# Optimization experiments

Hardware: AMD Instinct MI355X
Metric: run time of the kernel (lower is better)

## Reference

```python
import jax, jax.numpy as jnp
import numpy as np

RADIUS = 3.0  # suppression radius in meters (init kwarg `radius`)


def _radius_nms(x, y, valid, radius):
    """Greedy radius NMS over points in index order.
    x, y: [N] coordinates; valid: [N] bool (point belongs to this class).
    Returns keep mask [N]: point kept iff valid and not within `radius` of
    any previously kept point.
    """
    N = x.shape[0]
    r2 = radius * radius

    def step(supp, i):
        keep = valid[i] & jnp.logical_not(supp[i])
        d2 = (x - x[i]) ** 2 + (y - y[i]) ** 2  # [N]
        supp = supp | (keep & (d2 <= r2))
        return supp, keep

    _, keeps = jax.lax.scan(step, jnp.zeros(N, dtype=bool), jnp.arange(N))
    return keeps


def setup_inputs() -> dict:
    key = jax.random.key(0)
    k1, k2 = jax.random.split(key)
    B, C, W, H, CL = 4, 4, 64, 128, 5
    segmented_channels = jax.random.normal(k1, (B, C, W, H), dtype=jnp.float32)
    # lidar channels 0,1 are x,y point coordinates (meters); scale for realism
    lidar = jax.random.normal(k2, (B, CL, W, H), dtype=jnp.float32) * 30.0
    return {"segmented_channels": segmented_channels, "lidar": lidar}


def reference(segmented_channels, lidar):
    B, C, W, H = segmented_channels.shape
    N = W * H
    # val, ind = segmented_channels.max(dim=1) -> per-pixel predicted class
    ind = jnp.argmax(segmented_channels, axis=1).reshape(B, N)  # [B, N] int
    x = lidar[:, 0].reshape(B, N)  # [B, N]
    y = lidar[:, 1].reshape(B, N)
    # classes 1 .. C-1 (class 0 = background, skipped in the loop)
    classes = jnp.arange(1, C)
    valid = ind[:, None, :] == classes[None, :, None]  # [B, C-1, N] bool
    # vmap greedy NMS over classes, then over batch (x,y shared across classes)
    nms_c = jax.vmap(_radius_nms, in_axes=(None, None, 0, None))
    nms_bc = jax.vmap(nms_c, in_axes=(0, 0, 0, None))
    keep = nms_bc(x, y, valid, RADIUS)  # [B, C-1, N] bool
    # dense (padded) stand-in for the ragged per-class kept point lists:
    # kept coordinates where keep, zeros elsewhere
    coords = jnp.stack([x, y], axis=-1)  # [B, N, 2]
    kept_coords = coords[:, None, :, :] * keep[..., None].astype(coords.dtype)  # [B, C-1, N, 2]
    return kept_coords, keep
```

## Files before the change

kernel.cpp:

```cpp
#include <hip/hip_runtime.h>
#include <cstdint>


#define NPTS 8192
#define CAP  2560
#define R2C  9.0f
#define GW   60
#define GORG 126.0f
#define GINV 0.23809524f
#define GMAXC 59.0f

__global__ __launch_bounds__(1024) void radius_nms_kernel(
    const float* __restrict__ seg,
    const float* __restrict__ lidar,
    float* __restrict__ out)
{
#pragma clang fp contract(off)
    const int bx   = blockIdx.x;
    const int b    = bx / 3;
    const int cls  = (bx % 3) + 1;
    const int tid  = threadIdx.x;
    const int lane = tid & 63;
    const int wv   = tid >> 6;

    __shared__ float2 xy[CAP + 1];
    __shared__ unsigned short oidx[CAP];
    __shared__ unsigned long long keptW[CAP / 64];
    __shared__ int waveTot[16];
    __shared__ unsigned short slots[GW * GW * 4];
    __shared__ unsigned int cnt32[(GW * GW + 3) / 4];

    float* out0 = out + (size_t)bx * NPTS * 2;
    float* out1 = out + 196608 + (size_t)bx * NPTS;

    for (int i = tid; i < NPTS * 2; i += 1024) out0[i] = 0.0f;
    for (int i = tid; i < NPTS; i += 1024) out1[i] = 0.0f;
    for (int i = tid; i < GW * GW * 2; i += 1024)
        ((unsigned*)slots)[i] = ((unsigned)CAP << 16) | (unsigned)CAP;
    for (int i = tid; i < (GW * GW + 3) / 4; i += 1024) cnt32[i] = 0u;
    if (tid == 0) xy[CAP] = make_float2(3.0e38f, 3.0e38f);

    const float* segb = seg + (size_t)b * 4 * NPTS;
    const float* lx   = lidar + (size_t)b * 5 * NPTS;
    const float* ly   = lx + NPTS;

    float px[8], py[8];
    int flags = 0, cnt = 0;
    const int n0 = tid * 8;
#pragma unroll
    for (int k = 0; k < 8; ++k) {
        const int n = n0 + k;
        float v0 = segb[n];
        float v1 = segb[NPTS + n];
        float v2 = segb[2 * NPTS + n];
        float v3 = segb[3 * NPTS + n];
        int bi = 0; float bv = v0;
        if (v1 > bv) { bv = v1; bi = 1; }
        if (v2 > bv) { bv = v2; bi = 2; }
        if (v3 > bv) { bv = v3; bi = 3; }
        px[k] = lx[n];
        py[k] = ly[n];
        if (bi == cls) { flags |= (1 << k); ++cnt; }
    }

    int v = cnt;
    for (int off = 1; off < 64; off <<= 1) {
        int nv = __shfl_up(v, off, 64);
        if (lane >= off) v += nv;
    }
    if (lane == 63) waveTot[wv] = v;
    __syncthreads();
    if (wv == 0) {
        int t = (lane < 16) ? waveTot[lane] : 0;
        for (int off = 1; off < 16; off <<= 1) {
            int nt = __shfl_up(t, off, 64);
            if (lane >= off) t += nt;
        }
        if (lane < 16) waveTot[lane] = t;
    }
    __syncthreads();

    int M = waveTot[15];
    if (M > CAP) M = CAP;
    int base = ((wv == 0) ? 0 : waveTot[wv - 1]) + v - cnt;
#pragma unroll
    for (int k = 0; k < 8; ++k) {
        if (flags & (1 << k)) {
            if (base < CAP) {
                xy[base] = make_float2(px[k], py[k]);
                oidx[base] = (unsigned short)(n0 + k);
            }
            ++base;
        }
    }
    __syncthreads();

    if (wv == 0) {
        const int ntiles = (M + 63) >> 6;
        for (int t = 0; t < ntiles; ++t) {
            const int ts = t << 6;
            const int p  = ts + lane;
            float qx = 3.0e38f, qy = 3.0e38f;
            if (p < M) { float2 q = xy[p]; qx = q.x; qy = q.y; }

            float fx = floorf((qx + GORG) * GINV);
            fx = fminf(fmaxf(fx, 0.0f), GMAXC);
            float fy = floorf((qy + GORG) * GINV);
            fy = fminf(fmaxf(fy, 0.0f), GMAXC);
            const int cx = (int)fx, cy = (int)fy;

            const int cxm = (cx > 0) ? cx - 1 : 0;
            const int cxp = (cx < GW - 1) ? cx + 1 : GW - 1;
            const int rm  = ((cy > 0) ? cy - 1 : 0) * GW;
            const int r0  = cy * GW;
            const int rp  = ((cy < GW - 1) ? cy + 1 : GW - 1) * GW;

            unsigned long long sw[9];
            sw[0] = *(const unsigned long long*)&slots[(rm + cxm) * 4];
            sw[1] = *(const unsigned long long*)&slots[(rm + cx ) * 4];
            sw[2] = *(const unsigned long long*)&slots[(rm + cxp) * 4];
            sw[3] = *(const unsigned long long*)&slots[(r0 + cxm) * 4];
            sw[4] = *(const unsigned long long*)&slots[(r0 + cx ) * 4];
            sw[5] = *(const unsigned long long*)&slots[(r0 + cxp) * 4];
            sw[6] = *(const unsigned long long*)&slots[(rp + cxm) * 4];
            sw[7] = *(const unsigned long long*)&slots[(rp + cx ) * 4];
            sw[8] = *(const unsigned long long*)&slots[(rp + cxp) * 4];

            bool sup = false;
#pragma unroll
            for (int i = 0; i < 9; ++i) {
                unsigned long long w = sw[i];
#pragma unroll
                for (int k = 0; k < 4; ++k) {
                    int idx = (int)((w >> (16 * k)) & 0xFFFFull);
                    float2 r = xy[idx];
                    float dx = qx - r.x;
                    float dy = qy - r.y;
                    sup |= (dx * dx + dy * dy) <= R2C;
                }
            }

            int cntT = M - ts; if (cntT > 64) cntT = 64;
            unsigned long long tm =
                (cntT >= 64) ? ~0ull : ((1ull << cntT) - 1ull);
            unsigned long long alive = __ballot(!sup) & tm;
            unsigned long long keepm = 0ull;
            while (alive) {
                const int l = __builtin_ctzll(alive);
                const float xl = __int_as_float(
                    __builtin_amdgcn_readlane(__float_as_int(qx), l));
                const float yl = __int_as_float(
                    __builtin_amdgcn_readlane(__float_as_int(qy), l));
                const float dx = qx - xl;
                const float dy = qy - yl;
                unsigned long long b2 = __ballot((dx * dx + dy * dy) <= R2C);
                keepm |= (1ull << l);
                alive &= ~b2;
            }
            if (lane == 0) keptW[t] = keepm;

            if ((keepm >> lane) & 1ull) {
                const int c = cy * GW + cx;
                const unsigned sh = 8u * (unsigned)(c & 3);
                unsigned old = atomicAdd(&cnt32[c >> 2], 1u << sh);
                unsigned mc = (old >> sh) & 0xFFu;
                if (mc < 4u) slots[c * 4 + (int)mc] = (unsigned short)p;
            }
        }
    }
    __syncthreads();

    for (int j = tid; j < M; j += 1024) {
        if ((keptW[j >> 6] >> (j & 63)) & 1ull) {
            const int n = oidx[j];
            float2 q = xy[j];
            out0[2 * n]     = q.x;
            out0[2 * n + 1] = q.y;
            out1[n]         = 1.0f;
        }
    }
}

extern "C" void kernel_launch(void* const* d_in, const int* in_sizes, int n_in,
                              void* d_out, int out_size, void* d_ws, size_t ws_size,
                              hipStream_t stream) {
    const float* seg   = (const float*)d_in[0];
    const float* lidar = (const float*)d_in[1];
    float* out = (float*)d_out;
    radius_nms_kernel<<<dim3(12), dim3(1024), 0, stream>>>(seg, lidar, out);
}
```

Before: 121.0 us.

## Software-pipeline the grid NMS tile loop and vectorize loads with 512 threads

The serial single-wave tile loop is restructured so that the neighbor-slot lookups for the next tile are prefetched one iteration ahead. Suppression by the immediately preceding tile, whose points are not yet in the grid when the lookup happens, is checked directly against that tile's kept points through readlane. The block size drops to 512 threads, and the load and zero-fill phases use float4 accesses with 16 points per thread. This aims to hide LDS latency on the serial critical path and cut the number of memory instructions. In exchange it adds a per-tile loop over the previous tile's kept points and more register pressure.

```diff
diff --git a/kernel.cpp b/kernel.cpp
--- a/kernel.cpp
+++ b/kernel.cpp
@@ -10,7 +10,7 @@
 #define GINV 0.23809524f
 #define GMAXC 59.0f
 
-__global__ __launch_bounds__(1024) void radius_nms_kernel(
+__global__ __launch_bounds__(512) void radius_nms_kernel(
     const float* __restrict__ seg,
     const float* __restrict__ lidar,
     float* __restrict__ out)
@@ -26,41 +26,52 @@
     __shared__ float2 xy[CAP + 1];
     __shared__ unsigned short oidx[CAP];
     __shared__ unsigned long long keptW[CAP / 64];
-    __shared__ int waveTot[16];
+    __shared__ int waveTot[8];
     __shared__ unsigned short slots[GW * GW * 4];
     __shared__ unsigned int cnt32[(GW * GW + 3) / 4];
 
     float* out0 = out + (size_t)bx * NPTS * 2;
     float* out1 = out + 196608 + (size_t)bx * NPTS;
 
-    for (int i = tid; i < NPTS * 2; i += 1024) out0[i] = 0.0f;
-    for (int i = tid; i < NPTS; i += 1024) out1[i] = 0.0f;
-    for (int i = tid; i < GW * GW * 2; i += 1024)
+    {
+        float4 z = make_float4(0.f, 0.f, 0.f, 0.f);
+        float4* o0 = (float4*)out0;
+        float4* o1 = (float4*)out1;
+        for (int i = tid; i < NPTS / 2; i += 512) o0[i] = z;
+        for (int i = tid; i < NPTS / 4; i += 512) o1[i] = z;
+    }
+    for (int i = tid; i < GW * GW * 2; i += 512)
         ((unsigned*)slots)[i] = ((unsigned)CAP << 16) | (unsigned)CAP;
-    for (int i = tid; i < (GW * GW + 3) / 4; i += 1024) cnt32[i] = 0u;
+    for (int i = tid; i < (GW * GW + 3) / 4; i += 512) cnt32[i] = 0u;
     if (tid == 0) xy[CAP] = make_float2(3.0e38f, 3.0e38f);
+    if (tid < CAP / 64) keptW[tid] = 0ull;
 
     const float* segb = seg + (size_t)b * 4 * NPTS;
-    const float* lx   = lidar + (size_t)b * 5 * NPTS;
-    const float* ly   = lx + NPTS;
-
-    float px[8], py[8];
+    const float4* s4  = (const float4*)segb;
+    const float4* lx4 = (const float4*)(lidar + (size_t)b * 5 * NPTS);
+    const float4* ly4 = (const float4*)(lidar + (size_t)b * 5 * NPTS + NPTS);
+
+    float px[16], py[16];
     int flags = 0, cnt = 0;
-    const int n0 = tid * 8;
-#pragma unroll
-    for (int k = 0; k < 8; ++k) {
-        const int n = n0 + k;
-        float v0 = segb[n];
-        float v1 = segb[NPTS + n];
-        float v2 = segb[2 * NPTS + n];
-        float v3 = segb[3 * NPTS + n];
-        int bi = 0; float bv = v0;
-        if (v1 > bv) { bv = v1; bi = 1; }
-        if (v2 > bv) { bv = v2; bi = 2; }
-        if (v3 > bv) { bv = v3; bi = 3; }
-        px[k] = lx[n];
-        py[k] = ly[n];
-        if (bi == cls) { flags |= (1 << k); ++cnt; }
+    const int n0 = tid * 16;
+#pragma unroll
+    for (int g = 0; g < 4; ++g) {
+        const int vi = tid * 4 + g;
+        float4 v0 = s4[vi];
+        float4 v1 = s4[2048 + vi];
+        float4 v2 = s4[4096 + vi];
+        float4 v3 = s4[6144 + vi];
+        float4 X  = lx4[vi];
+        float4 Y  = ly4[vi];
+#define ELT(FLD, E) { \
+        int bi = 0; float bv = v0.FLD; \
+        if (v1.FLD > bv) { bv = v1.FLD; bi = 1; } \
+        if (v2.FLD > bv) { bv = v2.FLD; bi = 2; } \
+        if (v3.FLD > bv) { bv = v3.FLD; bi = 3; } \
+        px[g * 4 + E] = X.FLD; py[g * 4 + E] = Y.FLD; \
+        if (bi == cls) { flags |= 1 << (g * 4 + E); ++cnt; } }
+        ELT(x, 0) ELT(y, 1) ELT(z, 2) ELT(w, 3)
+#undef ELT
     }
 
     int v = cnt;
@@ -71,21 +82,21 @@
     if (lane == 63) waveTot[wv] = v;
     __syncthreads();
     if (wv == 0) {
-        int t = (lane < 16) ? waveTot[lane] : 0;
-        for (int off = 1; off < 16; off <<= 1) {
+        int t = (lane < 8) ? waveTot[lane] : 0;
+        for (int off = 1; off < 8; off <<= 1) {
             int nt = __shfl_up(t, off, 64);
             if (lane >= off) t += nt;
         }
-        if (lane < 16) waveTot[lane] = t;
-    }
-    __syncthreads();
-
-    int M = waveTot[15];
+        if (lane < 8) waveTot[lane] = t;
+    }
+    __syncthreads();
+
+    int M = waveTot[7];
     if (M > CAP) M = CAP;
     int base = ((wv == 0) ? 0 : waveTot[wv - 1]) + v - cnt;
 #pragma unroll
-    for (int k = 0; k < 8; ++k) {
-        if (flags & (1 << k)) {
+    for (int k = 0; k < 16; ++k) {
+        if ((flags >> k) & 1) {
             if (base < CAP) {
                 xy[base] = make_float2(px[k], py[k]);
                 oidx[base] = (unsigned short)(n0 + k);
@@ -96,49 +107,93 @@
     __syncthreads();
 
     if (wv == 0) {
+        auto cellOf = [&](float X, float Y, int& cx, int& cy) {
+            float fx = floorf((X + GORG) * GINV);
+            fx = fminf(fmaxf(fx, 0.0f), GMAXC);
+            float fy = floorf((Y + GORG) * GINV);
+            fy = fminf(fmaxf(fy, 0.0f), GMAXC);
+            cx = (int)fx; cy = (int)fy;
+        };
+
+        float qx, qy, q1x, q1y, pX = 0.f, pY = 0.f;
+        int cx0, cy0, cx1, cy1;
+        unsigned long long swc[9];
+        unsigned long long pKeep = 0ull;
+
+        {
+            int i0 = (lane < M) ? lane : CAP;
+            float2 q0 = xy[i0];
+            qx = q0.x; qy = q0.y;
+            int i1 = (64 + lane < M) ? 64 + lane : CAP;
+            float2 qq = xy[i1];
+            q1x = qq.x; q1y = qq.y;
+            cellOf(qx, qy, cx0, cy0);
+            const unsigned long long SEN = 0x0A000A000A000A00ull;
+#pragma unroll
+            for (int w = 0; w < 9; ++w) swc[w] = SEN;
+        }
+
         const int ntiles = (M + 63) >> 6;
         for (int t = 0; t < ntiles; ++t) {
             const int ts = t << 6;
-            const int p  = ts + lane;
-            float qx = 3.0e38f, qy = 3.0e38f;
-            if (p < M) { float2 q = xy[p]; qx = q.x; qy = q.y; }
-
-            float fx = floorf((qx + GORG) * GINV);
-            fx = fminf(fmaxf(fx, 0.0f), GMAXC);
-            float fy = floorf((qy + GORG) * GINV);
-            fy = fminf(fmaxf(fy, 0.0f), GMAXC);
-            const int cx = (int)fx, cy = (int)fy;
-
-            const int cxm = (cx > 0) ? cx - 1 : 0;
-            const int cxp = (cx < GW - 1) ? cx + 1 : GW - 1;
-            const int rm  = ((cy > 0) ? cy - 1 : 0) * GW;
-            const int r0  = cy * GW;
-            const int rp  = ((cy < GW - 1) ? cy + 1 : GW - 1) * GW;
-
-            unsigned long long sw[9];
-            sw[0] = *(const unsigned long long*)&slots[(rm + cxm) * 4];
-            sw[1] = *(const unsigned long long*)&slots[(rm + cx ) * 4];
-            sw[2] = *(const unsigned long long*)&slots[(rm + cxp) * 4];
-            sw[3] = *(const unsigned long long*)&slots[(r0 + cxm) * 4];
-            sw[4] = *(const unsigned long long*)&slots[(r0 + cx ) * 4];
-            sw[5] = *(const unsigned long long*)&slots[(r0 + cxp) * 4];
-            sw[6] = *(const unsigned long long*)&slots[(rp + cxm) * 4];
-            sw[7] = *(const unsigned long long*)&slots[(rp + cx ) * 4];
-            sw[8] = *(const unsigned long long*)&slots[(rp + cxp) * 4];
-
-            bool sup = false;
-#pragma unroll
-            for (int i = 0; i < 9; ++i) {
-                unsigned long long w = sw[i];
+
+            int i2 = ts + 128 + lane;
+            i2 = (i2 < M) ? i2 : CAP;
+            float2 q2 = xy[i2];
+
+            float rx[36], ry[36];
+#pragma unroll
+            for (int w = 0; w < 9; ++w) {
+                unsigned long long sw = swc[w];
 #pragma unroll
                 for (int k = 0; k < 4; ++k) {
-                    int idx = (int)((w >> (16 * k)) & 0xFFFFull);
-                    float2 r = xy[idx];
-                    float dx = qx - r.x;
-                    float dy = qy - r.y;
-                    sup |= (dx * dx + dy * dy) <= R2C;
+                    int idx = (int)((sw >> (16 * k)) & 0xFFFFull);
+                    float2 rr = xy[idx];
+                    rx[w * 4 + k] = rr.x;
+                    ry[w * 4 + k] = rr.y;
                 }
             }
+
+            cellOf(q1x, q1y, cx1, cy1);
+            unsigned long long swn[9];
+            {
+                int cxm = (cx1 > 0) ? cx1 - 1 : 0;
+                int cxp = (cx1 < GW - 1) ? cx1 + 1 : GW - 1;
+                int rm  = ((cy1 > 0) ? cy1 - 1 : 0) * GW;
+                int r0  = cy1 * GW;
+                int rp  = ((cy1 < GW - 1) ? cy1 + 1 : GW - 1) * GW;
+                swn[0] = *(const unsigned long long*)&slots[(rm + cxm) * 4];
+                swn[1] = *(const unsigned long long*)&slots[(rm + cx1) * 4];
+                swn[2] = *(const unsigned long long*)&slots[(rm + cxp) * 4];
+                swn[3] = *(const unsigned long long*)&slots[(r0 + cxm) * 4];
+                swn[4] = *(const unsigned long long*)&slots[(r0 + cx1) * 4];
+                swn[5] = *(const unsigned long long*)&slots[(r0 + cxp) * 4];
+                swn[6] = *(const unsigned long long*)&slots[(rp + cxm) * 4];
+                swn[7] = *(const unsigned long long*)&slots[(rp + cx1) * 4];
+                swn[8] = *(const unsigned long long*)&slots[(rp + cxp) * 4];
+            }
+
+            float m = 1.0e30f;
+            unsigned long long pk = pKeep;
+            while (pk) {
+                const int l = __builtin_ctzll(pk);
+                pk &= pk - 1;
+                float bxx = __int_as_float(
+                    __builtin_amdgcn_readlane(__float_as_int(pX), l));
+                float byy = __int_as_float(
+                    __builtin_amdgcn_readlane(__float_as_int(pY), l));
+                float dx = qx - bxx;
+                float dy = qy - byy;
+                m = fminf(m, dx * dx + dy * dy);
+            }
+
+#pragma unroll
+            for (int j = 0; j < 36; ++j) {
+                float dx = qx - rx[j];
+                float dy = qy - ry[j];
+                m = fminf(m, dx * dx + dy * dy);
+            }
+            const bool sup = (m <= R2C);
 
             int cntT = M - ts; if (cntT > 64) cntT = 64;
             unsigned long long tm =
@@ -160,17 +215,25 @@
             if (lane == 0) keptW[t] = keepm;
 
             if ((keepm >> lane) & 1ull) {
-                const int c = cy * GW + cx;
+                const int c = cy0 * GW + cx0;
                 const unsigned sh = 8u * (unsigned)(c & 3);
                 unsigned old = atomicAdd(&cnt32[c >> 2], 1u << sh);
                 unsigned mc = (old >> sh) & 0xFFu;
-                if (mc < 4u) slots[c * 4 + (int)mc] = (unsigned short)p;
-            }
-        }
-    }
-    __syncthreads();
-
-    for (int j = tid; j < M; j += 1024) {
+                if (mc < 4u) slots[c * 4 + (int)mc] = (unsigned short)(ts + lane);
+            }
+
+            pKeep = keepm; pX = qx; pY = qy;
+            qx = q1x; qy = q1y;
+            q1x = q2.x; q1y = q2.y;
+            cx0 = cx1; cy0 = cy1;
+#pragma unroll
+            for (int w = 0; w < 9; ++w) swc[w] = swn[w];
+            __builtin_amdgcn_wave_barrier();
+        }
+    }
+    __syncthreads();
+
+    for (int j = tid; j < M; j += 512) {
         if ((keptW[j >> 6] >> (j & 63)) & 1ull) {
             const int n = oidx[j];
             float2 q = xy[j];
@@ -187,5 +250,5 @@
     const float* seg   = (const float*)d_in[0];
     const float* lidar = (const float*)d_in[1];
     float* out = (float*)d_out;
-    radius_nms_kernel<<<dim3(12), dim3(1024), 0, stream>>>(seg, lidar, out);
+    radius_nms_kernel<<<dim3(12), dim3(512), 0, stream>>>(seg, lidar, out);
 }
```

After: 154.4 us. +27.6%, slower.

## Precompute intra-tile adjacency bitmasks on helper waves to shorten serial greedy loop

Applied to the files above, without the earlier changes.

Waves 1..14 now precompute, for a group of up to 14 tiles, a 64x64 within-tile adjacency bitmask in shared memory. Wave 0 then resolves greedy suppression inside a tile with readlane of those rows instead of recomputing distances and ballots per kept point. It also prefetches the next tile's coordinates and switches the per-cell counters to 4-bit nibbles. Global loads and output zeroing are vectorised to float4. This adds per-group block barriers and some redundant adjacency work in exchange for a shorter serial critical path.

```diff
diff --git a/kernel.cpp b/kernel.cpp
--- a/kernel.cpp
+++ b/kernel.cpp
@@ -9,6 +9,9 @@
 #define GORG 126.0f
 #define GINV 0.23809524f
 #define GMAXC 59.0f
+#define GRPT 14
+
+typedef unsigned long long u64;
 
 __global__ __launch_bounds__(1024) void radius_nms_kernel(
     const float* __restrict__ seg,
@@ -25,42 +28,53 @@
 
     __shared__ float2 xy[CAP + 1];
     __shared__ unsigned short oidx[CAP];
-    __shared__ unsigned long long keptW[CAP / 64];
+    __shared__ u64 keptW[CAP / 64];
     __shared__ int waveTot[16];
     __shared__ unsigned short slots[GW * GW * 4];
-    __shared__ unsigned int cnt32[(GW * GW + 3) / 4];
+    __shared__ unsigned nib[(GW * GW + 7) / 8];
+    __shared__ u64 adjT[GRPT * 64];
 
     float* out0 = out + (size_t)bx * NPTS * 2;
     float* out1 = out + 196608 + (size_t)bx * NPTS;
 
-    for (int i = tid; i < NPTS * 2; i += 1024) out0[i] = 0.0f;
-    for (int i = tid; i < NPTS; i += 1024) out1[i] = 0.0f;
+    {
+        float4 z = make_float4(0.f, 0.f, 0.f, 0.f);
+        float4* o0 = (float4*)out0;
+        float4* o1 = (float4*)out1;
+        for (int i = tid; i < NPTS / 2; i += 1024) o0[i] = z;
+        for (int i = tid; i < NPTS / 4; i += 1024) o1[i] = z;
+    }
     for (int i = tid; i < GW * GW * 2; i += 1024)
         ((unsigned*)slots)[i] = ((unsigned)CAP << 16) | (unsigned)CAP;
-    for (int i = tid; i < (GW * GW + 3) / 4; i += 1024) cnt32[i] = 0u;
+    for (int i = tid; i < (GW * GW + 7) / 8; i += 1024) nib[i] = 0u;
     if (tid == 0) xy[CAP] = make_float2(3.0e38f, 3.0e38f);
-
-    const float* segb = seg + (size_t)b * 4 * NPTS;
-    const float* lx   = lidar + (size_t)b * 5 * NPTS;
-    const float* ly   = lx + NPTS;
+    if (tid < CAP / 64) keptW[tid] = 0ull;
+
+    const float4* s4  = (const float4*)(seg + (size_t)b * 4 * NPTS);
+    const float4* lx4 = (const float4*)(lidar + (size_t)b * 5 * NPTS);
+    const float4* ly4 = lx4 + NPTS / 4;
 
     float px[8], py[8];
     int flags = 0, cnt = 0;
     const int n0 = tid * 8;
 #pragma unroll
-    for (int k = 0; k < 8; ++k) {
-        const int n = n0 + k;
-        float v0 = segb[n];
-        float v1 = segb[NPTS + n];
-        float v2 = segb[2 * NPTS + n];
-        float v3 = segb[3 * NPTS + n];
-        int bi = 0; float bv = v0;
-        if (v1 > bv) { bv = v1; bi = 1; }
-        if (v2 > bv) { bv = v2; bi = 2; }
-        if (v3 > bv) { bv = v3; bi = 3; }
-        px[k] = lx[n];
-        py[k] = ly[n];
-        if (bi == cls) { flags |= (1 << k); ++cnt; }
+    for (int g = 0; g < 2; ++g) {
+        const int vi = tid * 2 + g;
+        float4 v0 = s4[vi];
+        float4 v1 = s4[2048 + vi];
+        float4 v2 = s4[4096 + vi];
+        float4 v3 = s4[6144 + vi];
+        float4 X  = lx4[vi];
+        float4 Y  = ly4[vi];
+#define ELT(FLD, E) { \
+        int bi = 0; float bv = v0.FLD; \
+        if (v1.FLD > bv) { bv = v1.FLD; bi = 1; } \
+        if (v2.FLD > bv) { bv = v2.FLD; bi = 2; } \
+        if (v3.FLD > bv) { bv = v3.FLD; bi = 3; } \
+        px[g * 4 + E] = X.FLD; py[g * 4 + E] = Y.FLD; \
+        if (bi == cls) { flags |= 1 << (g * 4 + E); ++cnt; } }
+        ELT(x, 0) ELT(y, 1) ELT(z, 2) ELT(w, 3)
+#undef ELT
     }
 
     int v = cnt;
@@ -85,7 +99,7 @@
     int base = ((wv == 0) ? 0 : waveTot[wv - 1]) + v - cnt;
 #pragma unroll
     for (int k = 0; k < 8; ++k) {
-        if (flags & (1 << k)) {
+        if ((flags >> k) & 1) {
             if (base < CAP) {
                 xy[base] = make_float2(px[k], py[k]);
                 oidx[base] = (unsigned short)(n0 + k);
@@ -95,80 +109,122 @@
     }
     __syncthreads();
 
-    if (wv == 0) {
-        const int ntiles = (M + 63) >> 6;
-        for (int t = 0; t < ntiles; ++t) {
-            const int ts = t << 6;
-            const int p  = ts + lane;
-            float qx = 3.0e38f, qy = 3.0e38f;
-            if (p < M) { float2 q = xy[p]; qx = q.x; qy = q.y; }
-
-            float fx = floorf((qx + GORG) * GINV);
-            fx = fminf(fmaxf(fx, 0.0f), GMAXC);
-            float fy = floorf((qy + GORG) * GINV);
-            fy = fminf(fmaxf(fy, 0.0f), GMAXC);
-            const int cx = (int)fx, cy = (int)fy;
-
-            const int cxm = (cx > 0) ? cx - 1 : 0;
-            const int cxp = (cx < GW - 1) ? cx + 1 : GW - 1;
-            const int rm  = ((cy > 0) ? cy - 1 : 0) * GW;
-            const int r0  = cy * GW;
-            const int rp  = ((cy < GW - 1) ? cy + 1 : GW - 1) * GW;
-
-            unsigned long long sw[9];
-            sw[0] = *(const unsigned long long*)&slots[(rm + cxm) * 4];
-            sw[1] = *(const unsigned long long*)&slots[(rm + cx ) * 4];
-            sw[2] = *(const unsigned long long*)&slots[(rm + cxp) * 4];
-            sw[3] = *(const unsigned long long*)&slots[(r0 + cxm) * 4];
-            sw[4] = *(const unsigned long long*)&slots[(r0 + cx ) * 4];
-            sw[5] = *(const unsigned long long*)&slots[(r0 + cxp) * 4];
-            sw[6] = *(const unsigned long long*)&slots[(rp + cxm) * 4];
-            sw[7] = *(const unsigned long long*)&slots[(rp + cx ) * 4];
-            sw[8] = *(const unsigned long long*)&slots[(rp + cxp) * 4];
-
-            bool sup = false;
-#pragma unroll
-            for (int i = 0; i < 9; ++i) {
-                unsigned long long w = sw[i];
-#pragma unroll
-                for (int k = 0; k < 4; ++k) {
-                    int idx = (int)((w >> (16 * k)) & 0xFFFFull);
-                    float2 r = xy[idx];
-                    float dx = qx - r.x;
-                    float dy = qy - r.y;
-                    sup |= (dx * dx + dy * dy) <= R2C;
-                }
-            }
-
-            int cntT = M - ts; if (cntT > 64) cntT = 64;
-            unsigned long long tm =
-                (cntT >= 64) ? ~0ull : ((1ull << cntT) - 1ull);
-            unsigned long long alive = __ballot(!sup) & tm;
-            unsigned long long keepm = 0ull;
-            while (alive) {
-                const int l = __builtin_ctzll(alive);
-                const float xl = __int_as_float(
-                    __builtin_amdgcn_readlane(__float_as_int(qx), l));
-                const float yl = __int_as_float(
-                    __builtin_amdgcn_readlane(__float_as_int(qy), l));
-                const float dx = qx - xl;
-                const float dy = qy - yl;
-                unsigned long long b2 = __ballot((dx * dx + dy * dy) <= R2C);
-                keepm |= (1ull << l);
-                alive &= ~b2;
-            }
-            if (lane == 0) keptW[t] = keepm;
-
-            if ((keepm >> lane) & 1ull) {
-                const int c = cy * GW + cx;
-                const unsigned sh = 8u * (unsigned)(c & 3);
-                unsigned old = atomicAdd(&cnt32[c >> 2], 1u << sh);
-                unsigned mc = (old >> sh) & 0xFFu;
-                if (mc < 4u) slots[c * 4 + (int)mc] = (unsigned short)p;
-            }
-        }
-    }
-    __syncthreads();
+    const int ntiles  = (M + 63) >> 6;
+    const int ngroups = (ntiles + GRPT - 1) / GRPT;
+
+    for (int g = 0; g < ngroups; ++g) {
+        const int t0 = g * GRPT;
+
+        if (wv >= 1 && wv <= GRPT) {
+            const int t = t0 + wv - 1;
+            if (t < ntiles) {
+                const int ts = t << 6;
+                const int p  = ts + lane;
+                float2 q = xy[(p < M) ? p : CAP];
+                u64 row = 0ull;
+#pragma unroll
+                for (int j = 0; j < 64; j += 2) {
+                    float4 two = *(const float4*)&xy[ts + j];
+                    float dx0 = q.x - two.x, dy0 = q.y - two.y;
+                    float dx1 = q.x - two.z, dy1 = q.y - two.w;
+                    float s0 = dx0 * dx0 + dy0 * dy0;
+                    float s1 = dx1 * dx1 + dy1 * dy1;
+                    row |= ((u64)(s0 <= R2C)) << j;
+                    row |= ((u64)(s1 <= R2C)) << (j + 1);
+                }
+                adjT[(wv - 1) * 64 + lane] = row;
+            }
+        }
+        __syncthreads();
+
+        if (wv == 0) {
+            const int tEnd = (t0 + GRPT < ntiles) ? t0 + GRPT : ntiles;
+            int p0 = (t0 << 6) + lane;
+            float2 qq = xy[(p0 < M) ? p0 : CAP];
+            float qx = qq.x, qy = qq.y;
+            int cx, cy;
+            {
+                float fx = floorf((qx + GORG) * GINV);
+                fx = fminf(fmaxf(fx, 0.0f), GMAXC);
+                float fy = floorf((qy + GORG) * GINV);
+                fy = fminf(fmaxf(fy, 0.0f), GMAXC);
+                cx = (int)fx; cy = (int)fy;
+            }
+            for (int t = t0; t < tEnd; ++t) {
+                const int s  = t - t0;
+                const int ts = t << 6;
+
+                u64 row = adjT[s * 64 + lane];
+
+                const int cxm = (cx > 0) ? cx - 1 : 0;
+                const int cxp = (cx < GW - 1) ? cx + 1 : GW - 1;
+                const int rm  = ((cy > 0) ? cy - 1 : 0) * GW;
+                const int r0  = cy * GW;
+                const int rp  = ((cy < GW - 1) ? cy + 1 : GW - 1) * GW;
+                u64 sw[9];
+                sw[0] = *(const u64*)&slots[(rm + cxm) * 4];
+                sw[1] = *(const u64*)&slots[(rm + cx ) * 4];
+                sw[2] = *(const u64*)&slots[(rm + cxp) * 4];
+                sw[3] = *(const u64*)&slots[(r0 + cxm) * 4];
+                sw[4] = *(const u64*)&slots[(r0 + cx ) * 4];
+                sw[5] = *(const u64*)&slots[(r0 + cxp) * 4];
+                sw[6] = *(const u64*)&slots[(rp + cxm) * 4];
+                sw[7] = *(const u64*)&slots[(rp + cx ) * 4];
+                sw[8] = *(const u64*)&slots[(rp + cxp) * 4];
+
+                int pn = ((t + 1) << 6) + lane;
+                float2 qn = xy[(pn < M) ? pn : CAP];
+
+                float m = 1.0e30f;
+#pragma unroll
+                for (int w = 0; w < 9; ++w) {
+                    u64 sww = sw[w];
+#pragma unroll
+                    for (int k = 0; k < 4; ++k) {
+                        int idx = (int)((sww >> (16 * k)) & 0xFFFFull);
+                        float2 r = xy[idx];
+                        float dx = qx - r.x;
+                        float dy = qy - r.y;
+                        m = fminf(m, dx * dx + dy * dy);
+                    }
+                }
+                const bool sup = (m <= R2C);
+
+                int cntT = M - ts; if (cntT > 64) cntT = 64;
+                u64 tm = (cntT >= 64) ? ~0ull : ((1ull << cntT) - 1ull);
+                u64 alive = __ballot(!sup) & tm;
+                u64 keepm = 0ull;
+                const int rowLo = (int)(unsigned)row;
+                const int rowHi = (int)(unsigned)(row >> 32);
+                while (alive) {
+                    const int l = __builtin_ctzll(alive);
+                    unsigned rl = (unsigned)__builtin_amdgcn_readlane(rowLo, l);
+                    unsigned rh = (unsigned)__builtin_amdgcn_readlane(rowHi, l);
+                    keepm |= 1ull << l;
+                    alive &= ~(((u64)rh << 32) | (u64)rl);
+                }
+                if (lane == 0) keptW[t] = keepm;
+
+                if ((keepm >> lane) & 1ull) {
+                    const int c = cy * GW + cx;
+                    const unsigned sh = 4u * (unsigned)(c & 7);
+                    unsigned old = atomicAdd(&nib[c >> 3], 1u << sh);
+                    unsigned mc = (old >> sh) & 0xFu;
+                    if (mc < 4u) slots[c * 4 + (int)mc] = (unsigned short)(ts + lane);
+                }
+
+                qx = qn.x; qy = qn.y;
+                {
+                    float fx = floorf((qx + GORG) * GINV);
+                    fx = fminf(fmaxf(fx, 0.0f), GMAXC);
+                    float fy = floorf((qy + GORG) * GINV);
+                    fy = fminf(fmaxf(fy, 0.0f), GMAXC);
+                    cx = (int)fx; cy = (int)fy;
+                }
+            }
+        }
+        __syncthreads();
+    }
 
     for (int j = tid; j < M; j += 1024) {
         if ((keptW[j >> 6] >> (j & 63)) & 1ull) {
```

Measured after the change: 124.4 us. 1.03x slower.
